# Kernel optimization log

Hardware: AMD Instinct MI355X
Metric: run time of the kernel (lower is better)

Reference implementation:

```python
import jax, jax.numpy as jnp
import numpy as np

B = 8192
IN = 1024
H = 1024


def setup_inputs() -> dict:
    key = jax.random.key(0)
    ks = jax.random.split(key, 7)
    stdv = 1.0 / np.sqrt(H)
    u = lambda k, shape: jax.random.uniform(k, shape, jnp.float32, -stdv, stdv)
    return {
        "input": jax.random.normal(ks[0], (B, IN), jnp.float32),
        "h_prev": jax.random.normal(ks[1], (B, H), jnp.float32),
        "c_prev": jax.random.normal(ks[2], (B, H), jnp.float32),
        "W_ih": u(ks[3], (4 * H, IN)),
        "b_ih": u(ks[4], (4 * H,)),
        "W_hh": u(ks[5], (4 * H, H)),
        "b_hh": u(ks[6], (4 * H,)),
    }


def reference(input, h_prev, c_prev, W_ih, b_ih, W_hh, b_hh):
    # gates: [B, 4H] = input @ W_ih^T + b_ih + h_prev @ W_hh^T + b_hh
    gates = (jnp.einsum("bi,gi->bg", input, W_ih) + b_ih
             + jnp.einsum("bh,gh->bg", h_prev, W_hh) + b_hh)
    i_in, f_in, g_in, o_in = jnp.split(gates, 4, axis=1)
    i_t = jax.nn.sigmoid(i_in)
    f_t = jax.nn.sigmoid(f_in)
    g_t = jnp.tanh(g_in)
    o_t = jax.nn.sigmoid(o_in)
    c_t = f_t * c_prev + i_t * g_t
    h_t = o_t * jnp.tanh(c_t)
    return (h_t, c_t)
```

## Files before the change

kernel.cpp:

```cpp
#include <hip/hip_runtime.h>
#include <hip/hip_bf16.h>
#include <stdint.h>


typedef __attribute__((ext_vector_type(8))) __bf16 bf16x8;
typedef __attribute__((ext_vector_type(8))) unsigned short u16x8;
typedef __attribute__((ext_vector_type(4))) float f32x4;

__device__ __forceinline__ unsigned short f2bf(float f) {
  union { float f; unsigned int u; } v; v.f = f;
  unsigned int u = v.u;
  unsigned int r = u + 0x7FFFu + ((u >> 16) & 1u);
  return (unsigned short)(r >> 16);
}

__global__ void cvt_kernel(const float* __restrict__ src,
                           unsigned short* __restrict__ dst, int n4) {
  int i = blockIdx.x * blockDim.x + threadIdx.x;
  int stride = gridDim.x * blockDim.x;
  for (; i < n4; i += stride) {
    float4 v = ((const float4*)src)[i];
    ushort4 o;
    o.x = f2bf(v.x); o.y = f2bf(v.y); o.z = f2bf(v.z); o.w = f2bf(v.w);
    ((ushort4*)dst)[i] = o;
  }
}

#define GLOAD_LDS(gp, lofs)                                                    \
  __builtin_amdgcn_global_load_lds(                                            \
      (const __attribute__((address_space(1))) void*)(gp),                     \
      (__attribute__((address_space(3))) void*)(smem_raw + (lofs)), 16, 0, 0)

__global__ void lstm_fused(const unsigned short* __restrict__ Xb,
                           const unsigned short* __restrict__ Hb,
                           const unsigned short* __restrict__ Wihb,
                           const unsigned short* __restrict__ Whhb,
                           const float* __restrict__ bih,
                           const float* __restrict__ bhh,
                           const float* __restrict__ cprev,
                           float* __restrict__ out) {
  __shared__ __align__(16) char smem_raw[32768];
  unsigned short (*sA)[64] = (unsigned short (*)[64])smem_raw;
  unsigned short (*sB)[64] = (unsigned short (*)[64])(smem_raw + 16384);
  float (*eps)[128] = (float (*)[128])smem_raw;

  const int tid = threadIdx.x;
  const int lane = tid & 63;
  const int wid = tid >> 6;
  const int wr = wid >> 1;
  const int wc = wid & 1;
  const int l15 = lane & 15;
  const int l4 = lane >> 4;

  const int m0 = blockIdx.x * 128;
  const int h0 = blockIdx.y * 32;

  const int srow = tid >> 3;
  const int scol = (tid & 7) << 3;

  f32x4 acc[4][4];
#pragma unroll
  for (int m = 0; m < 4; ++m)
#pragma unroll
    for (int n = 0; n < 4; ++n) {
      f32x4 z = {0.f, 0.f, 0.f, 0.f};
      acc[m][n] = z;
    }

  for (int k0 = 0; k0 < 2048; k0 += 64) {
    const unsigned short* As = (k0 < 1024) ? Xb : Hb;
    const unsigned short* Bs = (k0 < 1024) ? Wihb : Whhb;
    const int kk = k0 & 1023;
#pragma unroll
    for (int p = 0; p < 4; ++p) {
      const unsigned short* ga =
          As + (size_t)(m0 + p * 32 + srow) * 1024 + kk + scol;
      GLOAD_LDS(ga, p * 4096 + wid * 1024);
      const unsigned short* gb =
          Bs + (size_t)(p * 1024 + h0 + srow) * 1024 + kk + scol;
      GLOAD_LDS(gb, 16384 + p * 4096 + wid * 1024);
    }
    __syncthreads();
#pragma unroll
    for (int kk2 = 0; kk2 < 2; ++kk2) {
      bf16x8 afr[4], bfr[4];
#pragma unroll
      for (int m = 0; m < 4; ++m) {
        u16x8 t = *(const u16x8*)&sA[wr * 64 + m * 16 + l15][kk2 * 32 + l4 * 8];
        afr[m] = __builtin_bit_cast(bf16x8, t);
      }
#pragma unroll
      for (int n = 0; n < 4; ++n) {
        u16x8 t = *(const u16x8*)&sB[wc * 64 + n * 16 + l15][kk2 * 32 + l4 * 8];
        bfr[n] = __builtin_bit_cast(bf16x8, t);
      }
#pragma unroll
      for (int m = 0; m < 4; ++m)
#pragma unroll
        for (int n = 0; n < 4; ++n)
          acc[m][n] = __builtin_amdgcn_mfma_f32_16x16x32_bf16(afr[m], bfr[n],
                                                              acc[m][n], 0, 0, 0);
    }
    __syncthreads();
  }

#pragma unroll
  for (int phase = 0; phase < 2; ++phase) {
    if (wr == phase) {
#pragma unroll
      for (int m = 0; m < 4; ++m)
#pragma unroll
        for (int n = 0; n < 4; ++n)
#pragma unroll
          for (int r = 0; r < 4; ++r)
            eps[m * 16 + l4 * 4 + r][wc * 64 + n * 16 + l15] = acc[m][n][r];
    }
    __syncthreads();
#pragma unroll
    for (int it = 0; it < 8; ++it) {
      int idx = it * 256 + tid;
      int h = idx & 31;
      int r = idx >> 5;
      int gh = h0 + h;
      size_t grow = (size_t)(m0 + phase * 64 + r);
      float vi = eps[r][h]       + bih[gh]         + bhh[gh];
      float vf = eps[r][32 + h]  + bih[1024 + gh]  + bhh[1024 + gh];
      float vg = eps[r][64 + h]  + bih[2048 + gh]  + bhh[2048 + gh];
      float vo = eps[r][96 + h]  + bih[3072 + gh]  + bhh[3072 + gh];
      float si = 1.f / (1.f + __expf(-vi));
      float sf = 1.f / (1.f + __expf(-vf));
      float tg = tanhf(vg);
      float so = 1.f / (1.f + __expf(-vo));
      float cp = cprev[grow * 1024 + gh];
      float ct = sf * cp + si * tg;
      float ht = so * tanhf(ct);
      out[grow * 1024 + gh] = ht;
      out[(size_t)8388608 + grow * 1024 + gh] = ct;
    }
    __syncthreads();
  }
}

extern "C" void kernel_launch(void* const* d_in, const int* in_sizes, int n_in,
                              void* d_out, int out_size, void* d_ws, size_t ws_size,
                              hipStream_t stream) {
  const float* input  = (const float*)d_in[0];
  const float* h_prev = (const float*)d_in[1];
  const float* c_prev = (const float*)d_in[2];
  const float* W_ih   = (const float*)d_in[3];
  const float* b_ih   = (const float*)d_in[4];
  const float* W_hh   = (const float*)d_in[5];
  const float* b_hh   = (const float*)d_in[6];
  float* out = (float*)d_out;

  unsigned short* Xb   = (unsigned short*)d_ws;
  unsigned short* Hb   = Xb + (size_t)8192 * 1024;
  unsigned short* Wihb = Hb + (size_t)8192 * 1024;
  unsigned short* Whhb = Wihb + (size_t)4096 * 1024;

  cvt_kernel<<<1024, 256, 0, stream>>>(input, Xb, 8192 * 1024 / 4);
  cvt_kernel<<<1024, 256, 0, stream>>>(h_prev, Hb, 8192 * 1024 / 4);
  cvt_kernel<<<512, 256, 0, stream>>>(W_ih, Wihb, 4096 * 1024 / 4);
  cvt_kernel<<<512, 256, 0, stream>>>(W_hh, Whhb, 4096 * 1024 / 4);

  dim3 grid(64, 32);
  lstm_fused<<<grid, 256, 0, stream>>>(Xb, Hb, Wihb, Whhb, b_ih, b_hh, c_prev, out);
}
```

Before: 346.8 us.

## Pre-swizzle bf16 operands during conversion to avoid LDS bank conflicts; merge cvt launches

```diff
diff --git a/kernel.cpp b/kernel.cpp
--- a/kernel.cpp
+++ b/kernel.cpp
@@ -14,15 +14,29 @@
   return (unsigned short)(r >> 16);
 }
 
-__global__ void cvt_kernel(const float* __restrict__ src,
-                           unsigned short* __restrict__ dst, int n4) {
+__global__ void cvt_swz(const float* __restrict__ s0, const float* __restrict__ s1,
+                        const float* __restrict__ s2, const float* __restrict__ s3,
+                        unsigned short* __restrict__ d0, unsigned short* __restrict__ d1,
+                        unsigned short* __restrict__ d2, unsigned short* __restrict__ d3) {
+  const float* src; unsigned short* dst; int nchunk;
+  if (blockIdx.y == 0)      { src = s0; dst = d0; nchunk = 8192 * 128; }
+  else if (blockIdx.y == 1) { src = s1; dst = d1; nchunk = 8192 * 128; }
+  else if (blockIdx.y == 2) { src = s2; dst = d2; nchunk = 4096 * 128; }
+  else                      { src = s3; dst = d3; nchunk = 4096 * 128; }
   int i = blockIdx.x * blockDim.x + threadIdx.x;
   int stride = gridDim.x * blockDim.x;
-  for (; i < n4; i += stride) {
-    float4 v = ((const float4*)src)[i];
-    ushort4 o;
-    o.x = f2bf(v.x); o.y = f2bf(v.y); o.z = f2bf(v.z); o.w = f2bf(v.w);
-    ((ushort4*)dst)[i] = o;
+  for (; i < nchunk; i += stride) {
+    int row = i >> 7;
+    int cw = i & 127;
+    int tile = cw >> 3;
+    int ct = cw & 7;
+    float4 a = ((const float4*)src)[i * 2];
+    float4 b = ((const float4*)src)[i * 2 + 1];
+    u16x8 o;
+    o[0] = f2bf(a.x); o[1] = f2bf(a.y); o[2] = f2bf(a.z); o[3] = f2bf(a.w);
+    o[4] = f2bf(b.x); o[5] = f2bf(b.y); o[6] = f2bf(b.z); o[7] = f2bf(b.w);
+    int oc = (row << 7) + (tile << 3) + (ct ^ (row & 7));
+    *(u16x8*)&dst[(size_t)oc * 8] = o;
   }
 }
 
@@ -86,12 +100,16 @@
       bf16x8 afr[4], bfr[4];
 #pragma unroll
       for (int m = 0; m < 4; ++m) {
-        u16x8 t = *(const u16x8*)&sA[wr * 64 + m * 16 + l15][kk2 * 32 + l4 * 8];
+        const int ra = wr * 64 + m * 16 + l15;
+        const int ca = ((kk2 * 4 + l4) ^ (ra & 7)) << 3;
+        u16x8 t = *(const u16x8*)&sA[ra][ca];
         afr[m] = __builtin_bit_cast(bf16x8, t);
       }
 #pragma unroll
       for (int n = 0; n < 4; ++n) {
-        u16x8 t = *(const u16x8*)&sB[wc * 64 + n * 16 + l15][kk2 * 32 + l4 * 8];
+        const int rb = wc * 64 + n * 16 + l15;
+        const int cb = ((kk2 * 4 + l4) ^ (rb & 7)) << 3;
+        u16x8 t = *(const u16x8*)&sB[rb][cb];
         bfr[n] = __builtin_bit_cast(bf16x8, t);
       }
 #pragma unroll
@@ -158,10 +176,8 @@
   unsigned short* Wihb = Hb + (size_t)8192 * 1024;
   unsigned short* Whhb = Wihb + (size_t)4096 * 1024;
 
-  cvt_kernel<<<1024, 256, 0, stream>>>(input, Xb, 8192 * 1024 / 4);
-  cvt_kernel<<<1024, 256, 0, stream>>>(h_prev, Hb, 8192 * 1024 / 4);
-  cvt_kernel<<<512, 256, 0, stream>>>(W_ih, Wihb, 4096 * 1024 / 4);
-  cvt_kernel<<<512, 256, 0, stream>>>(W_hh, Whhb, 4096 * 1024 / 4);
+  dim3 cgrid(1024, 4);
+  cvt_swz<<<cgrid, 256, 0, stream>>>(input, h_prev, W_ih, W_hh, Xb, Hb, Wihb, Whhb);
 
   dim3 grid(64, 32);
   lstm_fused<<<grid, 256, 0, stream>>>(Xb, Hb, Wihb, Whhb, b_ih, b_hh, c_prev, out);
```

After: 319.8 us. -7.8%, faster.
